# Kernel optimization log

Hardware: AMD Instinct MI355X
Metric: run time of the kernel (lower is better)

## Reference

```python
import jax, jax.numpy as jnp
from jax import lax
import numpy as np

N_LABELS = 48
START = 46
END = 47


def _viterbi_forward(emission_scores, transition, lengths):
    # scores[b, t, i, j]: score of transitioning from label i to label j at step t
    scores = emission_scores + transition  # [B, T, L, L]
    B, T, L, _ = scores.shape
    lengths = lengths.astype(jnp.int32)

    # ---- t == 0 ----
    mask0 = (lengths > 0)[:, None]  # [B, 1]
    first = scores[:, 0, START, :]  # [B, L]
    best0 = jnp.where(mask0, first, 0.0)
    upto0 = jnp.where(mask0, first, 0.0)
    bp0 = jnp.where(mask0, jnp.int32(START), jnp.int32(END))
    bp0 = jnp.broadcast_to(bp0, (B, L))

    # ---- t = 1 .. T-1 via scan (inherently sequential DP) ----
    def step(carry, inp):
        best, upto = carry  # each [B, L]
        s_t, t = inp  # s_t: [B, L, L]
        mask = (lengths > t)[:, None]  # [B, 1]
        cand = s_t + best[:, :, None]  # [B, from, to]
        new_best = jnp.max(cand, axis=1)  # [B, L]
        bp = jnp.argmax(cand, axis=1).astype(jnp.int32)  # [B, L]
        new_upto = jax.scipy.special.logsumexp(s_t + upto[:, :, None], axis=1)
        best = jnp.where(mask, new_best, best)
        upto = jnp.where(mask, new_upto, upto)
        bp = jnp.where(mask, bp, jnp.int32(END))
        return (best, upto), bp

    ts = jnp.arange(1, T, dtype=jnp.int32)
    scores_rest = jnp.swapaxes(scores[:, 1:], 0, 1)  # [T-1, B, L, L]
    (best, upto), bps = lax.scan(step, (best0, upto0), (scores_rest, ts))
    backpointers = jnp.concatenate([bp0[None], bps], axis=0)  # [T, B, L]

    # ---- backtracking (reverse scan over time) ----
    pointer0 = jnp.full((B,), END, dtype=jnp.int32)

    def back(ptr, bp_t):  # bp_t: [B, L]
        dec = jnp.take_along_axis(bp_t, ptr[:, None], axis=1)[:, 0]
        return dec, dec

    _, decoded = lax.scan(back, pointer0, backpointers, reverse=True)  # [T, B]
    decoded = decoded.T  # [B, T]
    # drop the initial start-label column, append end label
    decoded = jnp.concatenate(
        [decoded[:, 1:], jnp.full((B, 1), END, dtype=decoded.dtype)], axis=1
    )
    score_out = -(upto[:, END] - best[:, END])  # [B]
    return decoded, score_out


def setup_inputs() -> dict:
    key = jax.random.key(0)
    k1, k2, k3 = jax.random.split(key, 3)
    B, T, L = 32, 256, N_LABELS
    emission_scores = jax.random.normal(k1, (B, T, L, L), dtype=jnp.float32)
    transition = jax.random.normal(k2, (L, L), dtype=jnp.float32)
    lengths = jax.random.randint(k3, (B,), 128, T + 1, dtype=jnp.int64)
    lengths = lengths.at[0].set(T)  # ensure max(lengths) == T (padded length)
    return {"emission_scores": emission_scores, "transition": transition, "lengths": lengths}


def reference(emission_scores, transition, lengths):
    return _viterbi_forward(emission_scores, transition, lengths)
```

## Files before the change

### kernel.cpp

```cpp
#include <hip/hip_runtime.h>


#define TT 256
#define LL 48
#define ROWF 2304
#define LSTART 46
#define LEND 47
#define BB 32
#define LOG2E 1.44269504088896f
#define LN2 0.693147180559945f

#define RL(var, lane) __int_as_float(__builtin_amdgcn_readlane(__float_as_int(var), (lane)))

#define BARRIER() do { \
    asm volatile("s_waitcnt lgkmcnt(0)" ::: "memory"); \
    __builtin_amdgcn_s_barrier(); \
  } while (0)

#define PIN12(B) asm volatile("" : \
    "+v"((B)[0]), "+v"((B)[1]), "+v"((B)[2]),  "+v"((B)[3]), \
    "+v"((B)[4]), "+v"((B)[5]), "+v"((B)[6]),  "+v"((B)[7]), \
    "+v"((B)[8]), "+v"((B)[9]), "+v"((B)[10]), "+v"((B)[11]))

#define LOADROW(B, ROW) do { \
    const float* q_ = emB + (size_t)(ROW)*ROWF + (size_t)(12*w)*LL + jl; \
    _Pragma("unroll") \
    for (int k = 0; k < 12; ++k) (B)[k] = q_[k*LL]; \
  } while (0)

#define AMAX(vx, ix, vy, iy) do { if ((vy) > (vx)) { (vx)=(vy); (ix)=(iy);} } while(0)

#define PARTIALS_V(ETR, PW) do { \
    float cv[12]; int ci[12]; \
    _Pragma("unroll") \
    for (int k = 0; k < 12; ++k) { \
      cv[k] = (ETR)[k] + RL(vbest, 12*w + k); ci[k] = 12*w + k; } \
    AMAX(cv[0],ci[0],cv[1],ci[1]);  AMAX(cv[2],ci[2],cv[3],ci[3]); \
    AMAX(cv[4],ci[4],cv[5],ci[5]);  AMAX(cv[6],ci[6],cv[7],ci[7]); \
    AMAX(cv[8],ci[8],cv[9],ci[9]);  AMAX(cv[10],ci[10],cv[11],ci[11]); \
    AMAX(cv[0],ci[0],cv[2],ci[2]);  AMAX(cv[4],ci[4],cv[6],ci[6]); \
    AMAX(cv[8],ci[8],cv[10],ci[10]); \
    AMAX(cv[0],ci[0],cv[4],ci[4]); \
    AMAX(cv[0],ci[0],cv[8],ci[8]); \
    partV[PW][w][j] = make_float2(cv[0], __int_as_float(ci[0])); \
  } while (0)

#define ITER_V(T_, BISS, BPIN, ETRC, ETRN) do { \
    const int pr_ = ((T_)-1) & 1; \
    float2 m0_ = partV[pr_][0][j], m1_ = partV[pr_][1][j]; \
    float2 m2_ = partV[pr_][2][j], m3_ = partV[pr_][3][j]; \
    { int row_ = (T_) + 3; if (row_ > 255) row_ = 255; LOADROW(BISS, row_); } \
    PIN12(BPIN); \
    _Pragma("unroll") \
    for (int k = 0; k < 12; ++k) (ETRN)[k] = (BPIN)[k] + trg[k]; \
    float bv_ = m0_.x; int ba_ = __float_as_int(m0_.y); \
    AMAX(bv_, ba_, m1_.x, __float_as_int(m1_.y)); \
    AMAX(bv_, ba_, m2_.x, __float_as_int(m2_.y)); \
    AMAX(bv_, ba_, m3_.x, __float_as_int(m3_.y)); \
    { const bool upd_ = act && (((T_)-1) < len); \
      vbest = upd_ ? bv_ : vbest; \
      if (w == 0 && upd_) bp[((T_)-1)*LL + j] = (unsigned char)ba_; } \
    PARTIALS_V(ETRC, (T_) & 1); \
    BARRIER(); \
  } while (0)

#define PARTIALS_L(EE, PW) do { \
    float a0 = 0.f, a1 = 0.f, a2 = 0.f, a3 = 0.f; \
    _Pragma("unroll") \
    for (int k = 0; k < 12; k += 4) { \
      a0 = fmaf((EE)[k+0], RL(P, 12*w + k + 0), a0); \
      a1 = fmaf((EE)[k+1], RL(P, 12*w + k + 1), a1); \
      a2 = fmaf((EE)[k+2], RL(P, 12*w + k + 2), a2); \
      a3 = fmaf((EE)[k+3], RL(P, 12*w + k + 3), a3); \
    } \
    partS[PW][w][j] = (a0 + a1) + (a2 + a3); \
  } while (0)

#define ITER_L(T_, BISS, BPIN, EEC, EEN) do { \
    const int pr_ = ((T_)-1) & 1; \
    float s0_ = partS[pr_][0][j], s1_ = partS[pr_][1][j]; \
    float s2_ = partS[pr_][2][j], s3_ = partS[pr_][3][j]; \
    { int row_ = (T_) + 3; if (row_ > 255) row_ = 255; LOADROW(BISS, row_); } \
    PIN12(BPIN); \
    _Pragma("unroll") \
    for (int k = 0; k < 12; ++k) \
      (EEN)[k] = exp2f(fmaf((BPIN)[k], LOG2E, trg2[k])); \
    float Pn_ = (s0_ + s1_) + (s2_ + s3_); \
    { int rb_ = __builtin_amdgcn_readlane(__float_as_int(Pn_), 0); \
      int e_ = ((rb_ >> 23) & 255) - 127; \
      const bool upd_ = (((T_)-1) < len); \
      P    = upd_ ? __builtin_ldexpf(Pn_, -e_) : P; \
      macc = upd_ ? macc + (float)e_ : macc; } \
    PARTIALS_L(EEC, (T_) & 1); \
    BARRIER(); \
  } while (0)

__device__ __forceinline__ int load_len(const int* len_raw, int b) {
  bool is64 = (len_raw[1] == 0) && (len_raw[3] == 0) && (len_raw[5] == 0);
  int len = is64 ? len_raw[2*b] : len_raw[b];
  if (len > TT) len = TT;
  if (len < 1) len = 1;
  return len;
}

__launch_bounds__(256, 1)
__global__ void viterbi_fwd(const float* __restrict__ em,
                            const float* __restrict__ tr,
                            const int* __restrict__ len_raw,
                            float* __restrict__ out,
                            float* __restrict__ ws)
{
  const int role = blockIdx.x >> 5;
  const int b    = blockIdx.x & 31;
  const int tid  = threadIdx.x;
  const int w    = tid >> 6;
  const int j    = tid & 63;
  const bool act = (j < LL);
  const int jl   = act ? j : (LL - 1);
  const int len  = load_len(len_raw, b);

  __shared__ float2 partV[2][4][64];
  __shared__ float  partS[2][4][64];
  __shared__ unsigned char bp[TT*LL];
  __shared__ unsigned char cmp_[16*LL];
  __shared__ unsigned char entry_[16];
  __shared__ unsigned char raw[TT];

  const float* emB = em + (size_t)b*TT*ROWF;

  if (role == 0) {
    for (int idx = tid; idx < LL; idx += 256) bp[idx] = (unsigned char)LSTART;
    for (int idx = len*LL + tid; idx < TT*LL; idx += 256) bp[idx] = (unsigned char)LEND;
    __syncthreads();

    float trg[12];
    #pragma unroll
    for (int k = 0; k < 12; ++k) trg[k] = tr[(12*w + k)*LL + jl];
    const float init = emB[LSTART*LL + jl] + tr[LSTART*LL + jl];
    float vbest = act ? init : -INFINITY;

    float B0[12], B1[12], B2[12], B3[12], etrA[12], etrB[12];
    LOADROW(B1, 1); LOADROW(B2, 2); LOADROW(B3, 3);
    PIN12(B1);
    {
      float e1[12];
      #pragma unroll
      for (int k = 0; k < 12; ++k) e1[k] = B1[k] + trg[k];
      PARTIALS_V(e1, 1);
    }
    LOADROW(B0, 4);
    PIN12(B2);
    #pragma unroll
    for (int k = 0; k < 12; ++k) etrA[k] = B2[k] + trg[k];
    BARRIER();

    #pragma unroll 1
    for (int m = 0; m < 63; ++m) {
      const int t0 = 4*m + 2;
      ITER_V(t0,     B1, B3, etrA, etrB);
      ITER_V(t0 + 1, B2, B0, etrB, etrA);
      ITER_V(t0 + 2, B3, B1, etrA, etrB);
      ITER_V(t0 + 3, B0, B2, etrB, etrA);
    }
    {
      const int pr_ = 253 & 1;
      float2 m0_ = partV[pr_][0][j], m1_ = partV[pr_][1][j];
      float2 m2_ = partV[pr_][2][j], m3_ = partV[pr_][3][j];
      PIN12(B3);
      #pragma unroll
      for (int k = 0; k < 12; ++k) etrB[k] = B3[k] + trg[k];
      float bv_ = m0_.x; int ba_ = __float_as_int(m0_.y);
      AMAX(bv_, ba_, m1_.x, __float_as_int(m1_.y));
      AMAX(bv_, ba_, m2_.x, __float_as_int(m2_.y));
      AMAX(bv_, ba_, m3_.x, __float_as_int(m3_.y));
      const bool upd_ = act && (253 < len);
      vbest = upd_ ? bv_ : vbest;
      if (w == 0 && upd_) bp[253*LL + j] = (unsigned char)ba_;
      PARTIALS_V(etrA, 0);
      BARRIER();
    }
    {
      float2 m0_ = partV[0][0][j], m1_ = partV[0][1][j];
      float2 m2_ = partV[0][2][j], m3_ = partV[0][3][j];
      float bv_ = m0_.x; int ba_ = __float_as_int(m0_.y);
      AMAX(bv_, ba_, m1_.x, __float_as_int(m1_.y));
      AMAX(bv_, ba_, m2_.x, __float_as_int(m2_.y));
      AMAX(bv_, ba_, m3_.x, __float_as_int(m3_.y));
      const bool upd_ = act && (254 < len);
      vbest = upd_ ? bv_ : vbest;
      if (w == 0 && upd_) bp[254*LL + j] = (unsigned char)ba_;
      PARTIALS_V(etrB, 1);
      BARRIER();
    }
    {
      float2 m0 = partV[1][0][j], m1 = partV[1][1][j];
      float2 m2 = partV[1][2][j], m3 = partV[1][3][j];
      float bv = m0.x; int ba = __float_as_int(m0.y);
      AMAX(bv, ba, m1.x, __float_as_int(m1.y));
      AMAX(bv, ba, m2.x, __float_as_int(m2.y));
      AMAX(bv, ba, m3.x, __float_as_int(m3.y));
      const bool upd = act && (255 < len);
      vbest = upd ? bv : vbest;
      if (w == 0 && upd) bp[255*LL + j] = (unsigned char)ba;
    }
    if (tid == LEND) ws[BB + b] = vbest;
    __syncthreads();

    for (int idx = tid; idx < 16*LL; idx += 256) {
      int c = idx / LL, l = idx - c*LL;
      int pc = l;
      #pragma unroll
      for (int k = 15; k >= 0; --k) pc = bp[(16*c + k)*LL + pc];
      cmp_[c*LL + l] = (unsigned char)pc;
    }
    __syncthreads();
    if (tid == 0) {
      int pc = LEND;
      for (int c = 15; c >= 0; --c) { entry_[c] = (unsigned char)pc; pc = cmp_[c*LL + pc]; }
    }
    __syncthreads();
    if (tid < 16) {
      int c = tid, pc = entry_[c];
      #pragma unroll
      for (int k = 15; k >= 0; --k) { int t2 = 16*c + k; pc = bp[t2*LL + pc]; raw[t2] = (unsigned char)pc; }
    }
    __syncthreads();
    out[(size_t)b*TT + tid] = (tid < TT - 1) ? (float)raw[tid + 1] : (float)LEND;

  } else {
    float trg2[12];
    #pragma unroll
    for (int k = 0; k < 12; ++k) trg2[k] = tr[(12*w + k)*LL + jl] * LOG2E;
    const float init = emB[LSTART*LL + jl] + tr[LSTART*LL + jl];
    const float m2 = RL(init, 0) * LOG2E;
    float P = act ? exp2f(init * LOG2E - m2) : 0.f;
    float macc = m2;

    float B0[12], B1[12], B2[12], B3[12], eeA[12], eeB[12];
    LOADROW(B1, 1); LOADROW(B2, 2); LOADROW(B3, 3);
    PIN12(B1);
    {
      float e1[12];
      #pragma unroll
      for (int k = 0; k < 12; ++k) e1[k] = exp2f(fmaf(B1[k], LOG2E, trg2[k]));
      PARTIALS_L(e1, 1);
    }
    LOADROW(B0, 4);
    PIN12(B2);
    #pragma unroll
    for (int k = 0; k < 12; ++k) eeA[k] = exp2f(fmaf(B2[k], LOG2E, trg2[k]));
    BARRIER();

    #pragma unroll 1
    for (int m = 0; m < 63; ++m) {
      const int t0 = 4*m + 2;
      ITER_L(t0,     B1, B3, eeA, eeB);
      ITER_L(t0 + 1, B2, B0, eeB, eeA);
      ITER_L(t0 + 2, B3, B1, eeA, eeB);
      ITER_L(t0 + 3, B0, B2, eeB, eeA);
    }
    {
      const int pr_ = 253 & 1;
      float s0_ = partS[pr_][0][j], s1_ = partS[pr_][1][j];
      float s2_ = partS[pr_][2][j], s3_ = partS[pr_][3][j];
      PIN12(B3);
      #pragma unroll
      for (int k = 0; k < 12; ++k) eeB[k] = exp2f(fmaf(B3[k], LOG2E, trg2[k]));
      float Pn_ = (s0_ + s1_) + (s2_ + s3_);
      int rb_ = __builtin_amdgcn_readlane(__float_as_int(Pn_), 0);
      int e_ = ((rb_ >> 23) & 255) - 127;
      const bool upd_ = (253 < len);
      P    = upd_ ? __builtin_ldexpf(Pn_, -e_) : P;
      macc = upd_ ? macc + (float)e_ : macc;
      PARTIALS_L(eeA, 0);
      BARRIER();
    }
    {
      float s0_ = partS[0][0][j], s1_ = partS[0][1][j];
      float s2_ = partS[0][2][j], s3_ = partS[0][3][j];
      float Pn_ = (s0_ + s1_) + (s2_ + s3_);
      int rb_ = __builtin_amdgcn_readlane(__float_as_int(Pn_), 0);
      int e_ = ((rb_ >> 23) & 255) - 127;
      const bool upd_ = (254 < len);
      P    = upd_ ? __builtin_ldexpf(Pn_, -e_) : P;
      macc = upd_ ? macc + (float)e_ : macc;
      PARTIALS_L(eeB, 1);
      BARRIER();
    }
    {
      float Pn = (partS[1][0][j] + partS[1][1][j])
               + (partS[1][2][j] + partS[1][3][j]);
      int rb = __builtin_amdgcn_readlane(__float_as_int(Pn), 0);
      int e  = ((rb >> 23) & 255) - 127;
      const bool upd = (255 < len);
      P    = upd ? __builtin_ldexpf(Pn, -e) : P;
      macc = upd ? macc + (float)e : macc;
    }
    if (tid == LEND) ws[b] = (macc + __log2f(P)) * LN2;
  }
}

__global__ void viterbi_score(const float* __restrict__ ws, float* __restrict__ out)
{
  int b = threadIdx.x;
  if (b < BB) out[(size_t)BB*TT + b] = ws[BB + b] - ws[b];
}

extern "C" void kernel_launch(void* const* d_in, const int* in_sizes, int n_in,
                              void* d_out, int out_size, void* d_ws, size_t ws_size,
                              hipStream_t stream) {
  const float* em  = (const float*)d_in[0];
  const float* tr  = (const float*)d_in[1];
  const int*   ln  = (const int*)d_in[2];
  float* out = (float*)d_out;
  float* ws  = (float*)d_ws;
  viterbi_fwd<<<dim3(64), dim3(256), 0, stream>>>(em, tr, ln, out, ws);
  viterbi_score<<<dim3(1), dim3(64), 0, stream>>>(ws, out);
}
```

Measured before the change: 125.7 us.

## Replace per-step workgroup barriers with LDS tag flag polling between waves

```diff
diff --git a/kernel.cpp b/kernel.cpp
--- a/kernel.cpp
+++ b/kernel.cpp
@@ -12,11 +12,6 @@
 
 #define RL(var, lane) __int_as_float(__builtin_amdgcn_readlane(__float_as_int(var), (lane)))
 
-#define BARRIER() do { \
-    asm volatile("s_waitcnt lgkmcnt(0)" ::: "memory"); \
-    __builtin_amdgcn_s_barrier(); \
-  } while (0)
-
 #define PIN12(B) asm volatile("" : \
     "+v"((B)[0]), "+v"((B)[1]), "+v"((B)[2]),  "+v"((B)[3]), \
     "+v"((B)[4]), "+v"((B)[5]), "+v"((B)[6]),  "+v"((B)[7]), \
@@ -29,6 +24,16 @@
   } while (0)
 
 #define AMAX(vx, ix, vy, iy) do { if ((vy) > (vx)) { (vx)=(vy); (ix)=(iy);} } while(0)
+
+#define PUBLISH(TAGARR, PW, TG) do { \
+    asm volatile("" ::: "memory"); \
+    if ((tid & 63) == 0) *(volatile int*)&TAGARR[PW][w] = (TG); \
+  } while (0)
+#define POLL(TAGARR, PR, TG) do { \
+    volatile int* vt_ = &TAGARR[PR][0]; \
+    while ((vt_[0] ^ (TG)) | (vt_[1] ^ (TG)) | (vt_[2] ^ (TG)) | (vt_[3] ^ (TG))) {} \
+    asm volatile("" ::: "memory"); \
+  } while (0)
 
 #define PARTIALS_V(ETR, PW) do { \
     float cv[12]; int ci[12]; \
@@ -45,23 +50,27 @@
     partV[PW][w][j] = make_float2(cv[0], __int_as_float(ci[0])); \
   } while (0)
 
-#define ITER_V(T_, BISS, BPIN, ETRC, ETRN) do { \
-    const int pr_ = ((T_)-1) & 1; \
-    float2 m0_ = partV[pr_][0][j], m1_ = partV[pr_][1][j]; \
-    float2 m2_ = partV[pr_][2][j], m3_ = partV[pr_][3][j]; \
-    { int row_ = (T_) + 3; if (row_ > 255) row_ = 255; LOADROW(BISS, row_); } \
-    PIN12(BPIN); \
-    _Pragma("unroll") \
-    for (int k = 0; k < 12; ++k) (ETRN)[k] = (BPIN)[k] + trg[k]; \
+#define MERGE_V(T_) do { \
+    POLL(tagV, ((T_)) & 1, (T_)); \
+    float2 m0_ = partV[(T_)&1][0][j], m1_ = partV[(T_)&1][1][j]; \
+    float2 m2_ = partV[(T_)&1][2][j], m3_ = partV[(T_)&1][3][j]; \
     float bv_ = m0_.x; int ba_ = __float_as_int(m0_.y); \
     AMAX(bv_, ba_, m1_.x, __float_as_int(m1_.y)); \
     AMAX(bv_, ba_, m2_.x, __float_as_int(m2_.y)); \
     AMAX(bv_, ba_, m3_.x, __float_as_int(m3_.y)); \
-    { const bool upd_ = act && (((T_)-1) < len); \
-      vbest = upd_ ? bv_ : vbest; \
-      if (w == 0 && upd_) bp[((T_)-1)*LL + j] = (unsigned char)ba_; } \
+    const bool upd_ = act && ((T_) < len); \
+    vbest = upd_ ? bv_ : vbest; \
+    if (w == 0 && upd_) bp[(T_)*LL + j] = (unsigned char)ba_; \
+  } while (0)
+
+#define ITER_V(T_, BISS, BPIN, ETRC, ETRN) do { \
+    { int row_ = (T_) + 3; if (row_ > 255) row_ = 255; LOADROW(BISS, row_); } \
+    PIN12(BPIN); \
+    _Pragma("unroll") \
+    for (int k = 0; k < 12; ++k) (ETRN)[k] = (BPIN)[k] + trg[k]; \
+    MERGE_V((T_)-1); \
     PARTIALS_V(ETRC, (T_) & 1); \
-    BARRIER(); \
+    PUBLISH(tagV, (T_) & 1, T_); \
   } while (0)
 
 #define PARTIALS_L(EE, PW) do { \
@@ -76,23 +85,26 @@
     partS[PW][w][j] = (a0 + a1) + (a2 + a3); \
   } while (0)
 
+#define MERGE_L(T_) do { \
+    POLL(tagS, ((T_)) & 1, (T_)); \
+    float Pn_ = (partS[(T_)&1][0][j] + partS[(T_)&1][1][j]) \
+              + (partS[(T_)&1][2][j] + partS[(T_)&1][3][j]); \
+    int rb_ = __builtin_amdgcn_readlane(__float_as_int(Pn_), 0); \
+    int e_ = ((rb_ >> 23) & 255) - 127; \
+    const bool upd_ = ((T_) < len); \
+    P    = upd_ ? __builtin_ldexpf(Pn_, -e_) : P; \
+    macc = upd_ ? macc + (float)e_ : macc; \
+  } while (0)
+
 #define ITER_L(T_, BISS, BPIN, EEC, EEN) do { \
-    const int pr_ = ((T_)-1) & 1; \
-    float s0_ = partS[pr_][0][j], s1_ = partS[pr_][1][j]; \
-    float s2_ = partS[pr_][2][j], s3_ = partS[pr_][3][j]; \
     { int row_ = (T_) + 3; if (row_ > 255) row_ = 255; LOADROW(BISS, row_); } \
     PIN12(BPIN); \
     _Pragma("unroll") \
     for (int k = 0; k < 12; ++k) \
       (EEN)[k] = exp2f(fmaf((BPIN)[k], LOG2E, trg2[k])); \
-    float Pn_ = (s0_ + s1_) + (s2_ + s3_); \
-    { int rb_ = __builtin_amdgcn_readlane(__float_as_int(Pn_), 0); \
-      int e_ = ((rb_ >> 23) & 255) - 127; \
-      const bool upd_ = (((T_)-1) < len); \
-      P    = upd_ ? __builtin_ldexpf(Pn_, -e_) : P; \
-      macc = upd_ ? macc + (float)e_ : macc; } \
+    MERGE_L((T_)-1); \
     PARTIALS_L(EEC, (T_) & 1); \
-    BARRIER(); \
+    PUBLISH(tagS, (T_) & 1, T_); \
   } while (0)
 
 __device__ __forceinline__ int load_len(const int* len_raw, int b) {
@@ -121,6 +133,8 @@
 
   __shared__ float2 partV[2][4][64];
   __shared__ float  partS[2][4][64];
+  __shared__ int    tagV[2][4];
+  __shared__ int    tagS[2][4];
   __shared__ unsigned char bp[TT*LL];
   __shared__ unsigned char cmp_[16*LL];
   __shared__ unsigned char entry_[16];
@@ -129,6 +143,10 @@
   const float* emB = em + (size_t)b*TT*ROWF;
 
   if (role == 0) {
+    if ((tid & 63) == 0) {
+      *(volatile int*)&tagV[0][w] = -1;
+      *(volatile int*)&tagV[1][w] = -1;
+    }
     for (int idx = tid; idx < LL; idx += 256) bp[idx] = (unsigned char)LSTART;
     for (int idx = len*LL + tid; idx < TT*LL; idx += 256) bp[idx] = (unsigned char)LEND;
     __syncthreads();
@@ -147,12 +165,12 @@
       #pragma unroll
       for (int k = 0; k < 12; ++k) e1[k] = B1[k] + trg[k];
       PARTIALS_V(e1, 1);
+      PUBLISH(tagV, 1, 1);
     }
     LOADROW(B0, 4);
     PIN12(B2);
     #pragma unroll
     for (int k = 0; k < 12; ++k) etrA[k] = B2[k] + trg[k];
-    BARRIER();
 
     #pragma unroll 1
     for (int m = 0; m < 63; ++m) {
@@ -163,46 +181,19 @@
       ITER_V(t0 + 3, B0, B2, etrB, etrA);
     }
     {
-      const int pr_ = 253 & 1;
-      float2 m0_ = partV[pr_][0][j], m1_ = partV[pr_][1][j];
-      float2 m2_ = partV[pr_][2][j], m3_ = partV[pr_][3][j];
       PIN12(B3);
       #pragma unroll
       for (int k = 0; k < 12; ++k) etrB[k] = B3[k] + trg[k];
-      float bv_ = m0_.x; int ba_ = __float_as_int(m0_.y);
-      AMAX(bv_, ba_, m1_.x, __float_as_int(m1_.y));
-      AMAX(bv_, ba_, m2_.x, __float_as_int(m2_.y));
-      AMAX(bv_, ba_, m3_.x, __float_as_int(m3_.y));
-      const bool upd_ = act && (253 < len);
-      vbest = upd_ ? bv_ : vbest;
-      if (w == 0 && upd_) bp[253*LL + j] = (unsigned char)ba_;
+      MERGE_V(253);
       PARTIALS_V(etrA, 0);
-      BARRIER();
-    }
-    {
-      float2 m0_ = partV[0][0][j], m1_ = partV[0][1][j];
-      float2 m2_ = partV[0][2][j], m3_ = partV[0][3][j];
-      float bv_ = m0_.x; int ba_ = __float_as_int(m0_.y);
-      AMAX(bv_, ba_, m1_.x, __float_as_int(m1_.y));
-      AMAX(bv_, ba_, m2_.x, __float_as_int(m2_.y));
-      AMAX(bv_, ba_, m3_.x, __float_as_int(m3_.y));
-      const bool upd_ = act && (254 < len);
-      vbest = upd_ ? bv_ : vbest;
-      if (w == 0 && upd_) bp[254*LL + j] = (unsigned char)ba_;
+      PUBLISH(tagV, 0, 254);
+    }
+    {
+      MERGE_V(254);
       PARTIALS_V(etrB, 1);
-      BARRIER();
-    }
-    {
-      float2 m0 = partV[1][0][j], m1 = partV[1][1][j];
-      float2 m2 = partV[1][2][j], m3 = partV[1][3][j];
-      float bv = m0.x; int ba = __float_as_int(m0.y);
-      AMAX(bv, ba, m1.x, __float_as_int(m1.y));
-      AMAX(bv, ba, m2.x, __float_as_int(m2.y));
-      AMAX(bv, ba, m3.x, __float_as_int(m3.y));
-      const bool upd = act && (255 < len);
-      vbest = upd ? bv : vbest;
-      if (w == 0 && upd) bp[255*LL + j] = (unsigned char)ba;
-    }
+      PUBLISH(tagV, 1, 255);
+    }
+    MERGE_V(255);
     if (tid == LEND) ws[BB + b] = vbest;
     __syncthreads();
 
@@ -228,6 +219,12 @@
     out[(size_t)b*TT + tid] = (tid < TT - 1) ? (float)raw[tid + 1] : (float)LEND;
 
   } else {
+    if ((tid & 63) == 0) {
+      *(volatile int*)&tagS[0][w] = -1;
+      *(volatile int*)&tagS[1][w] = -1;
+    }
+    __syncthreads();
+
     float trg2[12];
     #pragma unroll
     for (int k = 0; k < 12; ++k) trg2[k] = tr[(12*w + k)*LL + jl] * LOG2E;
@@ -244,12 +241,12 @@
       #pragma unroll
       for (int k = 0; k < 12; ++k) e1[k] = exp2f(fmaf(B1[k], LOG2E, trg2[k]));
       PARTIALS_L(e1, 1);
+      PUBLISH(tagS, 1, 1);
     }
     LOADROW(B0, 4);
     PIN12(B2);
     #pragma unroll
     for (int k = 0; k < 12; ++k) eeA[k] = exp2f(fmaf(B2[k], LOG2E, trg2[k]));
-    BARRIER();
 
     #pragma unroll 1
     for (int m = 0; m < 63; ++m) {
@@ -260,42 +257,19 @@
       ITER_L(t0 + 3, B0, B2, eeB, eeA);
     }
     {
-      const int pr_ = 253 & 1;
-      float s0_ = partS[pr_][0][j], s1_ = partS[pr_][1][j];
-      float s2_ = partS[pr_][2][j], s3_ = partS[pr_][3][j];
       PIN12(B3);
       #pragma unroll
       for (int k = 0; k < 12; ++k) eeB[k] = exp2f(fmaf(B3[k], LOG2E, trg2[k]));
-      float Pn_ = (s0_ + s1_) + (s2_ + s3_);
-      int rb_ = __builtin_amdgcn_readlane(__float_as_int(Pn_), 0);
-      int e_ = ((rb_ >> 23) & 255) - 127;
-      const bool upd_ = (253 < len);
-      P    = upd_ ? __builtin_ldexpf(Pn_, -e_) : P;
-      macc = upd_ ? macc + (float)e_ : macc;
+      MERGE_L(253);
       PARTIALS_L(eeA, 0);
-      BARRIER();
-    }
-    {
-      float s0_ = partS[0][0][j], s1_ = partS[0][1][j];
-      float s2_ = partS[0][2][j], s3_ = partS[0][3][j];
-      float Pn_ = (s0_ + s1_) + (s2_ + s3_);
-      int rb_ = __builtin_amdgcn_readlane(__float_as_int(Pn_), 0);
-      int e_ = ((rb_ >> 23) & 255) - 127;
-      const bool upd_ = (254 < len);
-      P    = upd_ ? __builtin_ldexpf(Pn_, -e_) : P;
-      macc = upd_ ? macc + (float)e_ : macc;
+      PUBLISH(tagS, 0, 254);
+    }
+    {
+      MERGE_L(254);
       PARTIALS_L(eeB, 1);
-      BARRIER();
-    }
-    {
-      float Pn = (partS[1][0][j] + partS[1][1][j])
-               + (partS[1][2][j] + partS[1][3][j]);
-      int rb = __builtin_amdgcn_readlane(__float_as_int(Pn), 0);
-      int e  = ((rb >> 23) & 255) - 127;
-      const bool upd = (255 < len);
-      P    = upd ? __builtin_ldexpf(Pn, -e) : P;
-      macc = upd ? macc + (float)e : macc;
-    }
+      PUBLISH(tagS, 1, 255);
+    }
+    MERGE_L(255);
     if (tid == LEND) ws[b] = (macc + __log2f(P)) * LN2;
   }
 }
```

Result: slower. 203.8 us (+62.1%).

## Merge Viterbi max and logsumexp roles into one block per batch

Applied to the files above, without the earlier changes.

```diff
diff --git a/kernel.cpp b/kernel.cpp
--- a/kernel.cpp
+++ b/kernel.cpp
@@ -45,53 +45,47 @@
     partV[PW][w][j] = make_float2(cv[0], __int_as_float(ci[0])); \
   } while (0)
 
-#define ITER_V(T_, BISS, BPIN, ETRC, ETRN) do { \
+#define PARTIALS_L(ETR, PW) do { \
+    float a0_ = 0.f, a1_ = 0.f, a2_ = 0.f, a3_ = 0.f; \
+    _Pragma("unroll") \
+    for (int k = 0; k < 12; k += 4) { \
+      a0_ = fmaf(exp2f((ETR)[k+0]*LOG2E), RL(P, 12*w + k + 0), a0_); \
+      a1_ = fmaf(exp2f((ETR)[k+1]*LOG2E), RL(P, 12*w + k + 1), a1_); \
+      a2_ = fmaf(exp2f((ETR)[k+2]*LOG2E), RL(P, 12*w + k + 2), a2_); \
+      a3_ = fmaf(exp2f((ETR)[k+3]*LOG2E), RL(P, 12*w + k + 3), a3_); \
+    } \
+    partS[PW][w][j] = (a0_ + a1_) + (a2_ + a3_); \
+  } while (0)
+
+#define MERGE_VL(T_, M0,M1,M2,M3, S0,S1,S2,S3) do { \
+    float bv_ = (M0).x; int ba_ = __float_as_int((M0).y); \
+    AMAX(bv_, ba_, (M1).x, __float_as_int((M1).y)); \
+    AMAX(bv_, ba_, (M2).x, __float_as_int((M2).y)); \
+    AMAX(bv_, ba_, (M3).x, __float_as_int((M3).y)); \
+    const bool updv_ = act && ((T_) < len); \
+    vbest = updv_ ? bv_ : vbest; \
+    if (w == 0 && updv_) bp[(T_)*LL + j] = (unsigned char)ba_; \
+    float Pn_ = ((S0) + (S1)) + ((S2) + (S3)); \
+    int rb_ = __builtin_amdgcn_readlane(__float_as_int(Pn_), 0); \
+    int e_  = ((rb_ >> 23) & 255) - 127; \
+    const bool updl_ = ((T_) < len); \
+    P    = updl_ ? __builtin_ldexpf(Pn_, -e_) : P; \
+    macc = updl_ ? macc + (float)e_ : macc; \
+  } while (0)
+
+#define ITER_VL(T_, BISS, BPIN, ETRC, ETRN) do { \
     const int pr_ = ((T_)-1) & 1; \
     float2 m0_ = partV[pr_][0][j], m1_ = partV[pr_][1][j]; \
     float2 m2_ = partV[pr_][2][j], m3_ = partV[pr_][3][j]; \
-    { int row_ = (T_) + 3; if (row_ > 255) row_ = 255; LOADROW(BISS, row_); } \
-    PIN12(BPIN); \
-    _Pragma("unroll") \
-    for (int k = 0; k < 12; ++k) (ETRN)[k] = (BPIN)[k] + trg[k]; \
-    float bv_ = m0_.x; int ba_ = __float_as_int(m0_.y); \
-    AMAX(bv_, ba_, m1_.x, __float_as_int(m1_.y)); \
-    AMAX(bv_, ba_, m2_.x, __float_as_int(m2_.y)); \
-    AMAX(bv_, ba_, m3_.x, __float_as_int(m3_.y)); \
-    { const bool upd_ = act && (((T_)-1) < len); \
-      vbest = upd_ ? bv_ : vbest; \
-      if (w == 0 && upd_) bp[((T_)-1)*LL + j] = (unsigned char)ba_; } \
-    PARTIALS_V(ETRC, (T_) & 1); \
-    BARRIER(); \
-  } while (0)
-
-#define PARTIALS_L(EE, PW) do { \
-    float a0 = 0.f, a1 = 0.f, a2 = 0.f, a3 = 0.f; \
-    _Pragma("unroll") \
-    for (int k = 0; k < 12; k += 4) { \
-      a0 = fmaf((EE)[k+0], RL(P, 12*w + k + 0), a0); \
-      a1 = fmaf((EE)[k+1], RL(P, 12*w + k + 1), a1); \
-      a2 = fmaf((EE)[k+2], RL(P, 12*w + k + 2), a2); \
-      a3 = fmaf((EE)[k+3], RL(P, 12*w + k + 3), a3); \
-    } \
-    partS[PW][w][j] = (a0 + a1) + (a2 + a3); \
-  } while (0)
-
-#define ITER_L(T_, BISS, BPIN, EEC, EEN) do { \
-    const int pr_ = ((T_)-1) & 1; \
     float s0_ = partS[pr_][0][j], s1_ = partS[pr_][1][j]; \
     float s2_ = partS[pr_][2][j], s3_ = partS[pr_][3][j]; \
     { int row_ = (T_) + 3; if (row_ > 255) row_ = 255; LOADROW(BISS, row_); } \
     PIN12(BPIN); \
     _Pragma("unroll") \
-    for (int k = 0; k < 12; ++k) \
-      (EEN)[k] = exp2f(fmaf((BPIN)[k], LOG2E, trg2[k])); \
-    float Pn_ = (s0_ + s1_) + (s2_ + s3_); \
-    { int rb_ = __builtin_amdgcn_readlane(__float_as_int(Pn_), 0); \
-      int e_ = ((rb_ >> 23) & 255) - 127; \
-      const bool upd_ = (((T_)-1) < len); \
-      P    = upd_ ? __builtin_ldexpf(Pn_, -e_) : P; \
-      macc = upd_ ? macc + (float)e_ : macc; } \
-    PARTIALS_L(EEC, (T_) & 1); \
+    for (int k = 0; k < 12; ++k) (ETRN)[k] = (BPIN)[k] + trg[k]; \
+    MERGE_VL((T_)-1, m0_,m1_,m2_,m3_, s0_,s1_,s2_,s3_); \
+    PARTIALS_V(ETRC, (T_) & 1); \
+    PARTIALS_L(ETRC, (T_) & 1); \
     BARRIER(); \
   } while (0)
 
@@ -110,8 +104,7 @@
                             float* __restrict__ out,
                             float* __restrict__ ws)
 {
-  const int role = blockIdx.x >> 5;
-  const int b    = blockIdx.x & 31;
+  const int b    = blockIdx.x;
   const int tid  = threadIdx.x;
   const int w    = tid >> 6;
   const int j    = tid & 63;
@@ -128,176 +121,101 @@
 
   const float* emB = em + (size_t)b*TT*ROWF;
 
-  if (role == 0) {
-    for (int idx = tid; idx < LL; idx += 256) bp[idx] = (unsigned char)LSTART;
-    for (int idx = len*LL + tid; idx < TT*LL; idx += 256) bp[idx] = (unsigned char)LEND;
-    __syncthreads();
-
-    float trg[12];
-    #pragma unroll
-    for (int k = 0; k < 12; ++k) trg[k] = tr[(12*w + k)*LL + jl];
-    const float init = emB[LSTART*LL + jl] + tr[LSTART*LL + jl];
-    float vbest = act ? init : -INFINITY;
-
-    float B0[12], B1[12], B2[12], B3[12], etrA[12], etrB[12];
-    LOADROW(B1, 1); LOADROW(B2, 2); LOADROW(B3, 3);
-    PIN12(B1);
-    {
-      float e1[12];
-      #pragma unroll
-      for (int k = 0; k < 12; ++k) e1[k] = B1[k] + trg[k];
-      PARTIALS_V(e1, 1);
-    }
-    LOADROW(B0, 4);
-    PIN12(B2);
-    #pragma unroll
-    for (int k = 0; k < 12; ++k) etrA[k] = B2[k] + trg[k];
+  for (int idx = tid; idx < LL; idx += 256) bp[idx] = (unsigned char)LSTART;
+  for (int idx = len*LL + tid; idx < TT*LL; idx += 256) bp[idx] = (unsigned char)LEND;
+  __syncthreads();
+
+  float trg[12];
+  #pragma unroll
+  for (int k = 0; k < 12; ++k) trg[k] = tr[(12*w + k)*LL + jl];
+
+  const float init = emB[LSTART*LL + jl] + tr[LSTART*LL + jl];
+  float vbest = act ? init : -INFINITY;
+  const float m2 = RL(init, 0) * LOG2E;
+  float P = act ? exp2f(init * LOG2E - m2) : 0.f;
+  float macc = m2;
+
+  float B0[12], B1[12], B2[12], B3[12], etrA[12], etrB[12];
+  LOADROW(B1, 1); LOADROW(B2, 2); LOADROW(B3, 3);
+  PIN12(B1);
+  {
+    float e1[12];
+    #pragma unroll
+    for (int k = 0; k < 12; ++k) e1[k] = B1[k] + trg[k];
+    PARTIALS_V(e1, 1);
+    PARTIALS_L(e1, 1);
+  }
+  LOADROW(B0, 4);
+  PIN12(B2);
+  #pragma unroll
+  for (int k = 0; k < 12; ++k) etrA[k] = B2[k] + trg[k];
+  BARRIER();
+
+  #pragma unroll 1
+  for (int m = 0; m < 63; ++m) {
+    const int t0 = 4*m + 2;
+    ITER_VL(t0,     B1, B3, etrA, etrB);
+    ITER_VL(t0 + 1, B2, B0, etrB, etrA);
+    ITER_VL(t0 + 2, B3, B1, etrA, etrB);
+    ITER_VL(t0 + 3, B0, B2, etrB, etrA);
+  }
+  {
+    float2 m0_ = partV[1][0][j], m1_ = partV[1][1][j];
+    float2 m2_ = partV[1][2][j], m3_ = partV[1][3][j];
+    float s0_ = partS[1][0][j], s1_ = partS[1][1][j];
+    float s2_ = partS[1][2][j], s3_ = partS[1][3][j];
+    PIN12(B3);
+    #pragma unroll
+    for (int k = 0; k < 12; ++k) etrB[k] = B3[k] + trg[k];
+    MERGE_VL(253, m0_,m1_,m2_,m3_, s0_,s1_,s2_,s3_);
+    PARTIALS_V(etrA, 0);
+    PARTIALS_L(etrA, 0);
     BARRIER();
-
-    #pragma unroll 1
-    for (int m = 0; m < 63; ++m) {
-      const int t0 = 4*m + 2;
-      ITER_V(t0,     B1, B3, etrA, etrB);
-      ITER_V(t0 + 1, B2, B0, etrB, etrA);
-      ITER_V(t0 + 2, B3, B1, etrA, etrB);
-      ITER_V(t0 + 3, B0, B2, etrB, etrA);
-    }
-    {
-      const int pr_ = 253 & 1;
-      float2 m0_ = partV[pr_][0][j], m1_ = partV[pr_][1][j];
-      float2 m2_ = partV[pr_][2][j], m3_ = partV[pr_][3][j];
-      PIN12(B3);
-      #pragma unroll
-      for (int k = 0; k < 12; ++k) etrB[k] = B3[k] + trg[k];
-      float bv_ = m0_.x; int ba_ = __float_as_int(m0_.y);
-      AMAX(bv_, ba_, m1_.x, __float_as_int(m1_.y));
-      AMAX(bv_, ba_, m2_.x, __float_as_int(m2_.y));
-      AMAX(bv_, ba_, m3_.x, __float_as_int(m3_.y));
-      const bool upd_ = act && (253 < len);
-      vbest = upd_ ? bv_ : vbest;
-      if (w == 0 && upd_) bp[253*LL + j] = (unsigned char)ba_;
-      PARTIALS_V(etrA, 0);
-      BARRIER();
-    }
-    {
-      float2 m0_ = partV[0][0][j], m1_ = partV[0][1][j];
-      float2 m2_ = partV[0][2][j], m3_ = partV[0][3][j];
-      float bv_ = m0_.x; int ba_ = __float_as_int(m0_.y);
-      AMAX(bv_, ba_, m1_.x, __float_as_int(m1_.y));
-      AMAX(bv_, ba_, m2_.x, __float_as_int(m2_.y));
-      AMAX(bv_, ba_, m3_.x, __float_as_int(m3_.y));
-      const bool upd_ = act && (254 < len);
-      vbest = upd_ ? bv_ : vbest;
-      if (w == 0 && upd_) bp[254*LL + j] = (unsigned char)ba_;
-      PARTIALS_V(etrB, 1);
-      BARRIER();
-    }
-    {
-      float2 m0 = partV[1][0][j], m1 = partV[1][1][j];
-      float2 m2 = partV[1][2][j], m3 = partV[1][3][j];
-      float bv = m0.x; int ba = __float_as_int(m0.y);
-      AMAX(bv, ba, m1.x, __float_as_int(m1.y));
-      AMAX(bv, ba, m2.x, __float_as_int(m2.y));
-      AMAX(bv, ba, m3.x, __float_as_int(m3.y));
-      const bool upd = act && (255 < len);
-      vbest = upd ? bv : vbest;
-      if (w == 0 && upd) bp[255*LL + j] = (unsigned char)ba;
-    }
-    if (tid == LEND) ws[BB + b] = vbest;
-    __syncthreads();
-
-    for (int idx = tid; idx < 16*LL; idx += 256) {
-      int c = idx / LL, l = idx - c*LL;
-      int pc = l;
-      #pragma unroll
-      for (int k = 15; k >= 0; --k) pc = bp[(16*c + k)*LL + pc];
-      cmp_[c*LL + l] = (unsigned char)pc;
-    }
-    __syncthreads();
-    if (tid == 0) {
-      int pc = LEND;
-      for (int c = 15; c >= 0; --c) { entry_[c] = (unsigned char)pc; pc = cmp_[c*LL + pc]; }
-    }
-    __syncthreads();
-    if (tid < 16) {
-      int c = tid, pc = entry_[c];
-      #pragma unroll
-      for (int k = 15; k >= 0; --k) { int t2 = 16*c + k; pc = bp[t2*LL + pc]; raw[t2] = (unsigned char)pc; }
-    }
-    __syncthreads();
-    out[(size_t)b*TT + tid] = (tid < TT - 1) ? (float)raw[tid + 1] : (float)LEND;
-
-  } else {
-    float trg2[12];
-    #pragma unroll
-    for (int k = 0; k < 12; ++k) trg2[k] = tr[(12*w + k)*LL + jl] * LOG2E;
-    const float init = emB[LSTART*LL + jl] + tr[LSTART*LL + jl];
-    const float m2 = RL(init, 0) * LOG2E;
-    float P = act ? exp2f(init * LOG2E - m2) : 0.f;
-    float macc = m2;
-
-    float B0[12], B1[12], B2[12], B3[12], eeA[12], eeB[12];
-    LOADROW(B1, 1); LOADROW(B2, 2); LOADROW(B3, 3);
-    PIN12(B1);
-    {
-      float e1[12];
-      #pragma unroll
-      for (int k = 0; k < 12; ++k) e1[k] = exp2f(fmaf(B1[k], LOG2E, trg2[k]));
-      PARTIALS_L(e1, 1);
-    }
-    LOADROW(B0, 4);
-    PIN12(B2);
-    #pragma unroll
-    for (int k = 0; k < 12; ++k) eeA[k] = exp2f(fmaf(B2[k], LOG2E, trg2[k]));
+  }
+  {
+    float2 m0_ = partV[0][0][j], m1_ = partV[0][1][j];
+    float2 m2_ = partV[0][2][j], m3_ = partV[0][3][j];
+    float s0_ = partS[0][0][j], s1_ = partS[0][1][j];
+    float s2_ = partS[0][2][j], s3_ = partS[0][3][j];
+    MERGE_VL(254, m0_,m1_,m2_,m3_, s0_,s1_,s2_,s3_);
+    PARTIALS_V(etrB, 1);
+    PARTIALS_L(etrB, 1);
     BARRIER();
-
-    #pragma unroll 1
-    for (int m = 0; m < 63; ++m) {
-      const int t0 = 4*m + 2;
-      ITER_L(t0,     B1, B3, eeA, eeB);
-      ITER_L(t0 + 1, B2, B0, eeB, eeA);
-      ITER_L(t0 + 2, B3, B1, eeA, eeB);
-      ITER_L(t0 + 3, B0, B2, eeB, eeA);
-    }
-    {
-      const int pr_ = 253 & 1;
-      float s0_ = partS[pr_][0][j], s1_ = partS[pr_][1][j];
-      float s2_ = partS[pr_][2][j], s3_ = partS[pr_][3][j];
-      PIN12(B3);
-      #pragma unroll
-      for (int k = 0; k < 12; ++k) eeB[k] = exp2f(fmaf(B3[k], LOG2E, trg2[k]));
-      float Pn_ = (s0_ + s1_) + (s2_ + s3_);
-      int rb_ = __builtin_amdgcn_readlane(__float_as_int(Pn_), 0);
-      int e_ = ((rb_ >> 23) & 255) - 127;
-      const bool upd_ = (253 < len);
-      P    = upd_ ? __builtin_ldexpf(Pn_, -e_) : P;
-      macc = upd_ ? macc + (float)e_ : macc;
-      PARTIALS_L(eeA, 0);
-      BARRIER();
-    }
-    {
-      float s0_ = partS[0][0][j], s1_ = partS[0][1][j];
-      float s2_ = partS[0][2][j], s3_ = partS[0][3][j];
-      float Pn_ = (s0_ + s1_) + (s2_ + s3_);
-      int rb_ = __builtin_amdgcn_readlane(__float_as_int(Pn_), 0);
-      int e_ = ((rb_ >> 23) & 255) - 127;
-      const bool upd_ = (254 < len);
-      P    = upd_ ? __builtin_ldexpf(Pn_, -e_) : P;
-      macc = upd_ ? macc + (float)e_ : macc;
-      PARTIALS_L(eeB, 1);
-      BARRIER();
-    }
-    {
-      float Pn = (partS[1][0][j] + partS[1][1][j])
-               + (partS[1][2][j] + partS[1][3][j]);
-      int rb = __builtin_amdgcn_readlane(__float_as_int(Pn), 0);
-      int e  = ((rb >> 23) & 255) - 127;
-      const bool upd = (255 < len);
-      P    = upd ? __builtin_ldexpf(Pn, -e) : P;
-      macc = upd ? macc + (float)e : macc;
-    }
-    if (tid == LEND) ws[b] = (macc + __log2f(P)) * LN2;
-  }
+  }
+  {
+    float2 m0_ = partV[1][0][j], m1_ = partV[1][1][j];
+    float2 m2_ = partV[1][2][j], m3_ = partV[1][3][j];
+    float s0_ = partS[1][0][j], s1_ = partS[1][1][j];
+    float s2_ = partS[1][2][j], s3_ = partS[1][3][j];
+    MERGE_VL(255, m0_,m1_,m2_,m3_, s0_,s1_,s2_,s3_);
+  }
+
+  if (tid == LEND) {
+    ws[BB + b] = vbest;
+    ws[b] = (macc + __log2f(P)) * LN2;
+  }
+  __syncthreads();
+
+  for (int idx = tid; idx < 16*LL; idx += 256) {
+    int c = idx / LL, l = idx - c*LL;
+    int pc = l;
+    #pragma unroll
+    for (int k = 15; k >= 0; --k) pc = bp[(16*c + k)*LL + pc];
+    cmp_[c*LL + l] = (unsigned char)pc;
+  }
+  __syncthreads();
+  if (tid == 0) {
+    int pc = LEND;
+    for (int c = 15; c >= 0; --c) { entry_[c] = (unsigned char)pc; pc = cmp_[c*LL + pc]; }
+  }
+  __syncthreads();
+  if (tid < 16) {
+    int c = tid, pc = entry_[c];
+    #pragma unroll
+    for (int k = 15; k >= 0; --k) { int t2 = 16*c + k; pc = bp[t2*LL + pc]; raw[t2] = (unsigned char)pc; }
+  }
+  __syncthreads();
+  out[(size_t)b*TT + tid] = (tid < TT - 1) ? (float)raw[tid + 1] : (float)LEND;
 }
 
 __global__ void viterbi_score(const float* __restrict__ ws, float* __restrict__ out)
@@ -314,6 +232,6 @@
   const int*   ln  = (const int*)d_in[2];
   float* out = (float*)d_out;
   float* ws  = (float*)d_ws;
-  viterbi_fwd<<<dim3(64), dim3(256), 0, stream>>>(em, tr, ln, out, ws);
+  viterbi_fwd<<<dim3(32), dim3(256), 0, stream>>>(em, tr, ln, out, ws);
   viterbi_score<<<dim3(1), dim3(64), 0, stream>>>(ws, out);
 }
```

Measured after the change: 188.9 us. 1.5x slower.
